# Performance work log

Measured on AMD Instinct MI355X. Metric: run time of the kernel, lower is better.

The kernel has to match this reference:

```python
import jax, jax.numpy as jnp
import numpy as np

P_TH, N_TH, K, NEGPOS = 0.35, 0.4, 10, 7
V0, V1 = 0.1, 0.2


def point_form(b):
    return jnp.concatenate([b[..., :2] - b[..., 2:] / 2, b[..., :2] + b[..., 2:] / 2], -1)


def decode(loc, priors):
    # standard SSD decode, returns cxcywh (point_form is applied by caller)
    cxcy = priors[..., :2] + loc[..., :2] * V0 * priors[..., 2:]
    wh = priors[..., 2:] * jnp.exp(loc[..., 2:] * V1)
    return jnp.concatenate([cxcy, wh], -1)


def jaccard(a, b):
    # a: [N,4], b: [M,4] corner form -> [N,M] IoU
    tl = jnp.maximum(a[:, None, :2], b[None, :, :2])
    br = jnp.minimum(a[:, None, 2:], b[None, :, 2:])
    wh = jnp.clip(br - tl, 0.0)
    inter = wh[..., 0] * wh[..., 1]
    aa = ((a[:, 2] - a[:, 0]) * (a[:, 3] - a[:, 1]))[:, None]
    ab = ((b[:, 2] - b[:, 0]) * (b[:, 3] - b[:, 1]))[None, :]
    return inter / (aa + ab - inter)


def encode(matched, priors):
    g_cxcy = ((matched[..., :2] + matched[..., 2:]) / 2 - priors[..., :2]) / (V0 * priors[..., 2:])
    g_wh = jnp.log((matched[..., 2:] - matched[..., :2]) / priors[..., 2:]) / V1
    return jnp.concatenate([g_cxcy, g_wh], -1)


def encode_landm(matched, priors):
    m = matched.reshape(matched.shape[:-1] + (5, 2))
    g = (m - priors[..., None, :2]) / (V0 * priors[..., None, 2:])
    return g.reshape(matched.shape[:-1] + (10,))


def match_one(truths, loc_single, priors):
    # sequential per-object topk selection with column invalidation (as in original match())
    A = priors.shape[0]
    O = truths.shape[0]
    dec_pf = point_form(decode(jax.lax.stop_gradient(loc_single), priors))
    iou_a = jaccard(truths, point_form(priors))  # [O, A]
    iou_p = jaccard(truths, dec_pf)              # [O, A]

    def step(carry, i):
        iou_a, iou_p = carry
        va, ia = jax.lax.top_k(iou_a[i], K)
        av = va > P_TH
        av = jnp.where(av.any(), av, jnp.arange(K) == 0)  # fallback: best anchor
        ma = jnp.zeros(A, jnp.int32).at[ia].add(av.astype(jnp.int32)) > 0
        iou_a = jnp.where(ma[None, :], -1.0, iou_a)
        iou_p = jnp.where(ma[None, :], -1.0, iou_p)
        vp, ip = jax.lax.top_k(iou_p[i], K)
        pv = vp > P_TH + 0.05
        mp = jnp.zeros(A, jnp.int32).at[ip].add(pv.astype(jnp.int32)) > 0
        iou_a = jnp.where(mp[None, :], -1.0, iou_a)
        iou_p = jnp.where(mp[None, :], -1.0, iou_p)
        return (iou_a, iou_p), (ia, av, ip, pv)

    (iou_a, iou_p), (ia, av, ip, pv) = jax.lax.scan(step, (iou_a, iou_p), jnp.arange(O))
    p_idx = jnp.concatenate([ia, ip], 1).reshape(-1)    # [O*2K]
    p_valid = jnp.concatenate([av, pv], 1).reshape(-1)  # [O*2K] bool
    maxv = jnp.maximum(iou_a, iou_p).max(0)             # max over cat(IoU_A, IoU_P)
    neg_mask = (maxv != -1.0) & (maxv < N_TH)
    pos_mask = jnp.zeros(A, jnp.int32).at[p_idx].add(p_valid.astype(jnp.int32)) > 0
    conf = jnp.full(A, -2.0)
    conf = jnp.where(pos_mask, 1.0, conf)
    conf = jnp.where(neg_mask, 0.0, conf)
    return p_idx, p_valid, conf


def _smooth_l1(d):
    ad = jnp.abs(d)
    return jnp.where(ad < 1.0, 0.5 * d * d, ad - 0.5)


def reference(loc_data, conf_data, landm_data, priors, targets):
    B, A, _ = loc_data.shape
    O = targets.shape[1]
    truths = targets[..., :4]
    landms = targets[..., 4:14]
    labels = targets[..., 14]

    p_idx, p_valid, conf = jax.vmap(match_one, in_axes=(0, 0, None))(truths, loc_data, priors)
    p_true = jnp.repeat(jnp.arange(O), 2 * K)  # object id per match slot

    gat = jax.vmap(lambda x, i: x[i])
    pri_sel = priors[p_idx]            # [B, P, 4]
    tru_sel = truths[:, p_true, :]     # [B, P, 4]
    landm_sel = landms[:, p_true, :]   # [B, P, 10]
    lab_sel = labels[:, p_true]        # [B, P]

    # localization loss
    loc_p = gat(loc_data, p_idx)                       # [B, P, 4]
    loc_t = encode(tru_sel, pri_sel)
    wf = p_valid.astype(loc_data.dtype)
    loss_l = jnp.sum(_smooth_l1(loc_p - loc_t) * wf[..., None])
    N = jnp.sum(p_valid)

    # landmark loss (only label==1 positives, first 6 landm dims)
    lvalid = p_valid & (lab_sel == 1.0)
    landm_p = gat(landm_data, p_idx)                   # [B, P, 6]
    landm_t = encode_landm(landm_sel, pri_sel)[..., :6]
    loss_landm = jnp.sum(_smooth_l1(landm_p - landm_t) * lvalid.astype(loc_data.dtype)[..., None])
    N1 = jnp.sum(lvalid)

    # classification with hard negative mining
    lse = jax.nn.logsumexp(conf_data, axis=-1)         # [B, A]
    pos = conf == 1.0
    n_pos = pos.sum(1)                                  # [B]
    loss_pos = jnp.sum((lse - conf_data[..., 1]) * pos)
    negc = conf == 0.0
    loss_c = lse - conf_data[..., 0]                    # CE with label 0
    masked = jnp.where(negc, loss_c, -jnp.inf)
    order = jnp.argsort(-masked, axis=1)
    rank = jnp.argsort(order, axis=1)
    neg_sel = (rank < (n_pos * NEGPOS)[:, None]) & negc
    loss_neg = jnp.sum(loss_c * neg_sel)
    loss_cls = loss_pos + loss_neg

    return loss_l / N, loss_cls / N, loss_landm / N1


def setup_inputs() -> dict:
    key = jax.random.key(0)
    ks = jax.random.split(key, 8)
    B, A, O = 16, 65536, 24
    loc_data = jax.random.normal(ks[0], (B, A, 4), jnp.float32) * 0.1
    conf_data = jax.random.normal(ks[1], (B, A, 2), jnp.float32)
    landm_data = jax.random.normal(ks[2], (B, A, 6), jnp.float32)
    # priors: cxcywh in unit square with positive wh
    pc = jax.random.uniform(ks[3], (A, 2), jnp.float32, 0.05, 0.95)
    pwh = jax.random.uniform(ks[4], (A, 2), jnp.float32, 0.02, 0.2)
    priors = jnp.concatenate([pc, pwh], 1)
    # targets: valid corner-form boxes + 10 landm coords + label 1
    tc = jax.random.uniform(ks[5], (B, O, 2), jnp.float32, 0.15, 0.85)
    twh = jax.random.uniform(ks[6], (B, O, 2), jnp.float32, 0.05, 0.25)
    boxes = jnp.concatenate([tc - twh / 2, tc + twh / 2], -1)
    lm = jax.random.uniform(ks[7], (B, O, 10), jnp.float32)
    lab = jnp.ones((B, O, 1), jnp.float32)
    targets = jnp.concatenate([boxes, lm, lab], -1)
    return {"loc_data": loc_data, "conf_data": conf_data, "landm_data": landm_data, "priors": priors, "targets": targets}
```

## Files before the change

### kernel.cpp

```cpp
#include <hip/hip_runtime.h>

#define A_N 65536
#define B_N 16
#define O_N 24
#define KEEP 512
#define SELCAP 2048
#define PF 4

typedef unsigned long long u64;

__device__ __forceinline__ float sl1(float d){
  float ad = fabsf(d);
  return ad < 1.0f ? 0.5f * d * d : ad - 0.5f;
}

__device__ __forceinline__ float iou_box(float ax1, float ay1, float ax2, float ay2,
                                         float bx1, float by1, float bx2, float by2){
  float tlx = fmaxf(ax1, bx1), tly = fmaxf(ay1, by1);
  float brx = fminf(ax2, bx2), bry = fminf(ay2, by2);
  float w = fmaxf(brx - tlx, 0.0f), h = fmaxf(bry - tly, 0.0f);
  float inter = w * h;
  float aa = (ax2 - ax1) * (ay2 - ay1);
  float ab = (bx2 - bx1) * (by2 - by1);
  return inter / (aa + ab - inter);
}

__global__ __launch_bounds__(256) void prep_kernel(const float* __restrict__ loc,
    const float* __restrict__ priors, float4* __restrict__ dec,
    float4* __restrict__ pf, unsigned char* __restrict__ flags){
  const int a = blockIdx.x * 256 + threadIdx.x;
  const int b = blockIdx.y;
  const float4 pr = ((const float4*)priors)[a];
  const float4 l = ((const float4*)loc)[(size_t)b * A_N + a];
  float cx = pr.x + l.x * 0.1f * pr.z;
  float cy = pr.y + l.y * 0.1f * pr.w;
  float w  = pr.z * expf(l.z * 0.2f);
  float h  = pr.w * expf(l.w * 0.2f);
  float4 d;
  d.x = cx - w * 0.5f; d.y = cy - h * 0.5f;
  d.z = cx + w * 0.5f; d.w = cy + h * 0.5f;
  dec[(size_t)b * A_N + a] = d;
  if (b == 0){
    float4 p;
    p.x = pr.x - pr.z * 0.5f; p.y = pr.y - pr.w * 0.5f;
    p.z = pr.x + pr.z * 0.5f; p.w = pr.y + pr.w * 0.5f;
    pf[a] = p;
  }
  flags[(size_t)b * A_N + a] = 0;
}

__device__ __forceinline__ void wave_sort_512(u64* sk, int base, int lane, bool asc){
  for (int k = 2; k <= 512; k <<= 1){
    for (int j = k >> 1; j > 0; j >>= 1){
      #pragma unroll
      for (int s = 0; s < 8; ++s){
        int t = lane + s * 64;
        int x = t ^ j;
        if (x > t){
          u64 ka = sk[base + t], kb = sk[base + x];
          bool up = (((t & k) == 0) != asc);
          bool sw = up ? (kb > ka) : (ka > kb);
          if (sw){ sk[base + t] = kb; sk[base + x] = ka; }
        }
      }
      __builtin_amdgcn_wave_barrier();
    }
  }
}

__global__ __launch_bounds__(256) void sel_kernel(const float4* __restrict__ dec,
    const float4* __restrict__ pf, const float* __restrict__ targets,
    unsigned char* __restrict__ flags,
    float* __restrict__ out_vals, int* __restrict__ out_idxs){
  __shared__ unsigned hist[2048];
  __shared__ u64 sk[SELCAP];
  __shared__ unsigned gsum_s[64];
  __shared__ int s_b1, s_cnt;
  const int r = blockIdx.x;
  const int type = r & 1;
  const int o = (r >> 1) % O_N;
  const int b = r / (O_N * 2);
  const int tid = threadIdx.x;
  const int w = tid >> 6;
  const int lane = tid & 63;
  const u64 lmask = (1ull << lane) - 1ull;
  const float* tg = targets + (size_t)(b * O_N + o) * 15;
  const float tx1 = tg[0], ty1 = tg[1], tx2 = tg[2], ty2 = tg[3];
  const float4* src = (type == 0) ? pf : (dec + (size_t)b * A_N);
  unsigned char* fl = flags + (size_t)b * A_N;

  for (int j = tid; j < 2048; j += 256) hist[j] = 0u;
  if (tid == 0) s_cnt = 0;
  __syncthreads();

  const int NCH = A_N / 256;
  {
    float4 nxt[PF];
    #pragma unroll
    for (int u = 0; u < PF; ++u) nxt[u] = src[u * 256 + tid];
    for (int c = 0; c < NCH; c += PF){
      float4 cur[PF];
      #pragma unroll
      for (int u = 0; u < PF; ++u) cur[u] = nxt[u];
      if (c + PF < NCH){
        #pragma unroll
        for (int u = 0; u < PF; ++u) nxt[u] = src[(c + PF + u) * 256 + tid];
      }
      #pragma unroll
      for (int u = 0; u < PF; ++u){
        const int a = (c + u) * 256 + tid;
        const float4 bb = cur[u];
        const float v = iou_box(tx1, ty1, tx2, ty2, bb.x, bb.y, bb.z, bb.w);
        if (v >= 0.4f) fl[a] = 1;
        if (v > 0.0f){
          unsigned bin = __float_as_uint(v) >> 19;
          if (bin > 2047u) bin = 2047u;
          atomicAdd(&hist[bin], 1u);
        }
      }
    }
  }
  __syncthreads();
  if (tid < 64){
    unsigned s = 0;
    #pragma unroll
    for (int e = 0; e < 32; ++e) s += hist[tid * 32 + e];
    gsum_s[tid] = s;
  }
  __syncthreads();
  if (tid == 0){
    int cum = 0, b1 = -1;
    for (int g = 63; g >= 0 && b1 < 0; --g){
      unsigned gs = gsum_s[g];
      if (cum + (int)gs >= KEEP){
        for (int bin = g * 32 + 31; bin >= g * 32; --bin){
          cum += (int)hist[bin];
          if (cum >= KEEP){ b1 = bin; break; }
        }
      } else cum += (int)gs;
    }
    s_b1 = (b1 < 0) ? 0 : b1;
  }
  __syncthreads();
  const int b1 = s_b1;
  {
    float4 nxt[PF];
    #pragma unroll
    for (int u = 0; u < PF; ++u) nxt[u] = src[u * 256 + tid];
    for (int c = 0; c < NCH; c += PF){
      float4 cur[PF];
      #pragma unroll
      for (int u = 0; u < PF; ++u) cur[u] = nxt[u];
      if (c + PF < NCH){
        #pragma unroll
        for (int u = 0; u < PF; ++u) nxt[u] = src[(c + PF + u) * 256 + tid];
      }
      #pragma unroll
      for (int u = 0; u < PF; ++u){
        const int a = (c + u) * 256 + tid;
        const float4 bb = cur[u];
        const float v = iou_box(tx1, ty1, tx2, ty2, bb.x, bb.y, bb.z, bb.w);
        unsigned bits = __float_as_uint(v);
        unsigned bin = bits >> 19;
        if (bin > 2047u) bin = 2047u;
        bool acc = (v > 0.0f) && ((int)bin >= b1);
        u64 m = __ballot(acc);
        if (m){
          int base = 0;
          if (lane == 0) base = atomicAdd(&s_cnt, (int)__popcll(m));
          base = __shfl(base, 0);
          if (acc){
            int p = base + (int)__popcll(m & lmask);
            if (p < SELCAP) sk[p] = ((u64)bits << 32) | (u64)(~(unsigned)a);
          }
        }
      }
    }
  }
  __syncthreads();
  int cnt = s_cnt; if (cnt > SELCAP) cnt = SELCAP;
  for (int j = cnt + tid; j < SELCAP; j += 256) sk[j] = 0ull;
  __syncthreads();
  wave_sort_512(sk, w * 512, lane, (w & 1) != 0);
  __syncthreads();
  for (int k = 1024; k <= 2048; k <<= 1){
    for (int j = k >> 1; j > 0; j >>= 1){
      for (int t = tid; t < SELCAP; t += 256){
        int x = t ^ j;
        if (x > t){
          u64 ka = sk[t], kb = sk[x];
          bool up = ((t & k) == 0);
          bool sw = up ? (kb > ka) : (ka > kb);
          if (sw){ sk[t] = kb; sk[x] = ka; }
        }
      }
      __syncthreads();
    }
  }
  for (int jj = tid; jj < KEEP; jj += 256){
    u64 kk = sk[jj];
    out_vals[(size_t)r * KEEP + jj] = __uint_as_float((unsigned)(kk >> 32));
    out_idxs[(size_t)r * KEEP + jj] = (kk == 0ull) ? 0 : (int)(~(unsigned)kk);
  }
}

__global__ __launch_bounds__(64) void scan_kernel(const float* __restrict__ vals,
    const int* __restrict__ idxs, int* __restrict__ p_idx, int* __restrict__ p_valid,
    unsigned int* __restrict__ bitset_g, int* __restrict__ n_pos_g){
  __shared__ unsigned int bs[A_N / 32];
  __shared__ float pv0[48][64];
  __shared__ int pi0[48][64];
  __shared__ float s_v[10];
  __shared__ int s_i[10];
  const int b = blockIdx.x;
  const int lane = threadIdx.x;
  for (int j = lane; j < A_N / 32; j += 64) bs[j] = 0u;
  for (int row = 0; row < 48; ++row){
    pv0[row][lane] = vals[(size_t)(b * 48 + row) * KEEP + lane];
    pi0[row][lane] = idxs[(size_t)(b * 48 + row) * KEEP + lane];
  }
  __syncthreads();
  int npos = 0;
  const float PTH2 = (float)(0.35 + 0.05);
  for (int o = 0; o < O_N; ++o){
    for (int ph = 0; ph < 2; ++ph){
      const int row48 = o * 2 + ph;
      const int r = b * 48 + row48;
      const float* rv = vals + (size_t)r * KEEP;
      const int* ri = idxs + (size_t)r * KEEP;
      int found = 0;
      for (int pos = 0; pos < KEEP && found < 10; pos += 64){
        float v; int id;
        if (pos == 0){ v = pv0[row48][lane]; id = pi0[row48][lane]; }
        else { v = rv[pos + lane]; id = ri[pos + lane]; }
        bool unm = ((bs[id >> 5] >> (id & 31)) & 1u) == 0u;
        unsigned long long m = __ballot(unm);
        int rank = found + __popcll(m & ((1ull << lane) - 1ull));
        if (unm && rank < 10){ s_v[rank] = v; s_i[rank] = id; }
        int add = __popcll(m);
        found = (found + add > 10) ? 10 : (found + add);
        __syncthreads();
      }
      if (lane == 0){
        const float th = (ph == 0) ? 0.35f : PTH2;
        float fv[10]; int fi[10]; int vv[10];
        bool any = false;
        for (int j = 0; j < 10; ++j){
          fv[j] = (j < found) ? s_v[j] : 0.0f;
          fi[j] = (j < found) ? s_i[j] : 0;
          vv[j] = (fv[j] > th) ? 1 : 0;
          any = any || (vv[j] != 0);
        }
        if (ph == 0 && !any) vv[0] = 1;
        int base_slot = b * (O_N * 20) + o * 20 + ph * 10;
        for (int j = 0; j < 10; ++j){
          p_idx[base_slot + j] = fi[j];
          p_valid[base_slot + j] = vv[j];
          if (vv[j]){
            bs[fi[j] >> 5] |= (1u << (fi[j] & 31));
            npos++;
          }
        }
      }
      __syncthreads();
    }
  }
  for (int j = lane; j < A_N / 32; j += 64) bitset_g[b * (A_N / 32) + j] = bs[j];
  if (lane == 0) n_pos_g[b] = npos;
}

__global__ __launch_bounds__(256) void anchor_kernel(const float* __restrict__ conf,
    const unsigned char* __restrict__ flags, const unsigned int* __restrict__ bitset_g,
    float* __restrict__ lossc, float* __restrict__ partial){
  const int b = blockIdx.y;
  const int a = blockIdx.x * 256 + threadIdx.x;
  __shared__ float red[256];
  bool masked = ((bitset_g[b * (A_N / 32) + (a >> 5)] >> (a & 31)) & 1u) != 0u;
  const float2 c = ((const float2*)conf)[(size_t)b * A_N + a];
  float mx = fmaxf(c.x, c.y);
  float lse = mx + log1pf(expf(-fabsf(c.x - c.y)));
  float lp = 0.0f;
  float lc = -1.0f;
  if (masked) lp = lse - c.y;
  else if (!flags[(size_t)b * A_N + a]) lc = lse - c.x;
  lossc[(size_t)b * A_N + a] = lc;
  red[threadIdx.x] = lp; __syncthreads();
  for (int s = 128; s > 0; s >>= 1){
    if (threadIdx.x < s) red[threadIdx.x] += red[threadIdx.x + s];
    __syncthreads();
  }
  if (threadIdx.x == 0) partial[blockIdx.y * gridDim.x + blockIdx.x] = red[0];
}

__global__ __launch_bounds__(512) void mine_kernel(const float* __restrict__ lossc,
    const int* __restrict__ n_pos_g, double* __restrict__ accum){
  __shared__ unsigned hist[8192];
  __shared__ u64 sk[SELCAP];
  __shared__ unsigned gsum_s[256];
  __shared__ int s_b1, s_need, s_cnt;
  __shared__ float red[512];
  const int b = blockIdx.x;
  const int tid = threadIdx.x;
  const int w = tid >> 6;
  const int lane = tid & 63;
  const u64 lmask = (1ull << lane) - 1ull;
  const float4* lc4 = (const float4*)(lossc + (size_t)b * A_N);
  const int M = n_pos_g[b] * 7;
  if (M <= 0) return;
  for (int j = tid; j < 8192; j += 512) hist[j] = 0u;
  if (tid == 0) s_cnt = 0;
  __syncthreads();
  for (int q = tid; q < A_N / 4; q += 512){
    float4 v4 = lc4[q];
    float vv[4] = {v4.x, v4.y, v4.z, v4.w};
    #pragma unroll
    for (int e = 0; e < 4; ++e){
      if (vv[e] >= 0.0f){
        unsigned bin = __float_as_uint(vv[e]) >> 19;
        if (bin > 8191u) bin = 8191u;
        atomicAdd(&hist[bin], 1u);
      }
    }
  }
  __syncthreads();
  if (tid < 256){
    unsigned s = 0;
    #pragma unroll
    for (int e = 0; e < 32; ++e) s += hist[tid * 32 + e];
    gsum_s[tid] = s;
  }
  __syncthreads();
  if (tid == 0){
    int cum = 0, b1 = -1, need = 0;
    for (int g = 255; g >= 0 && b1 < 0; --g){
      unsigned gs = gsum_s[g];
      if (cum + (int)gs >= M){
        for (int bin = g * 32 + 31; bin >= g * 32; --bin){
          int cc = (int)hist[bin];
          if (cum + cc >= M){ b1 = bin; need = M - cum; break; }
          cum += cc;
        }
      } else cum += (int)gs;
    }
    s_b1 = b1;
    s_need = need;
  }
  __syncthreads();
  const int b1 = s_b1;
  const int need = s_need;
  float sum = 0.0f;
  for (int q = tid; q < A_N / 4; q += 512){
    float4 v4 = lc4[q];
    float vv[4] = {v4.x, v4.y, v4.z, v4.w};
    #pragma unroll
    for (int e = 0; e < 4; ++e){
      float v = vv[e];
      bool isneg = (v >= 0.0f);
      unsigned bits = __float_as_uint(v);
      unsigned bin = bits >> 19;
      if (bin > 8191u) bin = 8191u;
      if (isneg && (int)bin > b1) sum += v;
      bool acc = isneg && ((int)bin == b1);
      u64 m = __ballot(acc);
      if (m){
        int base = 0;
        if (lane == 0) base = atomicAdd(&s_cnt, (int)__popcll(m));
        base = __shfl(base, 0);
        if (acc){
          int p = base + (int)__popcll(m & lmask);
          if (p < SELCAP) sk[p] = (u64)bits;
        }
      }
    }
  }
  __syncthreads();
  int cnt = s_cnt; if (cnt > SELCAP) cnt = SELCAP;
  for (int j = cnt + tid; j < SELCAP; j += 512) sk[j] = 0ull;
  __syncthreads();
  if (w < 4) wave_sort_512(sk, w * 512, lane, (w & 1) != 0);
  __syncthreads();
  for (int k = 1024; k <= 2048; k <<= 1){
    for (int j = k >> 1; j > 0; j >>= 1){
      for (int t = tid; t < SELCAP; t += 512){
        int x = t ^ j;
        if (x > t){
          u64 ka = sk[t], kb = sk[x];
          bool up = ((t & k) == 0);
          bool sw = up ? (kb > ka) : (ka > kb);
          if (sw){ sk[t] = kb; sk[x] = ka; }
        }
      }
      __syncthreads();
    }
  }
  for (int i = tid; i < need; i += 512) sum += __uint_as_float((unsigned)sk[i]);
  red[tid] = sum; __syncthreads();
  for (int s = 256; s > 0; s >>= 1){
    if (tid < s) red[tid] += red[tid + s];
    __syncthreads();
  }
  if (tid == 0) atomicAdd(&accum[3], (double)red[0]);
}

__global__ __launch_bounds__(512) void loss_lm_kernel(const float* __restrict__ loc,
    const float* __restrict__ landm, const float* __restrict__ priors,
    const float* __restrict__ targets, const int* __restrict__ p_idx,
    const int* __restrict__ p_valid, double* __restrict__ accum, int* __restrict__ cnts){
  const int b = blockIdx.x;
  const int j = threadIdx.x;
  float ll = 0.0f, lmv = 0.0f;
  int nv = 0, nv1 = 0;
  if (j < 480){
    int valid = p_valid[b * 480 + j];
    if (valid){
      int pid = p_idx[b * 480 + j];
      int t = j / 20;
      const float* tg = targets + (size_t)(b * O_N + t) * 15;
      float4 pr = ((const float4*)priors)[pid];
      float4 lp = ((const float4*)loc)[(size_t)b * A_N + pid];
      float gcx = ((tg[0] + tg[2]) * 0.5f - pr.x) / (0.1f * pr.z);
      float gcy = ((tg[1] + tg[3]) * 0.5f - pr.y) / (0.1f * pr.w);
      float gw = logf((tg[2] - tg[0]) / pr.z) / 0.2f;
      float gh = logf((tg[3] - tg[1]) / pr.w) / 0.2f;
      ll = sl1(lp.x - gcx) + sl1(lp.y - gcy) + sl1(lp.z - gw) + sl1(lp.w - gh);
      nv = 1;
      if (tg[14] == 1.0f){
        nv1 = 1;
        const float* lmp = landm + ((size_t)b * A_N + pid) * 6;
        for (int k = 0; k < 3; ++k){
          float gx = (tg[4 + 2 * k] - pr.x) / (0.1f * pr.z);
          float gy = (tg[5 + 2 * k] - pr.y) / (0.1f * pr.w);
          lmv += sl1(lmp[2 * k] - gx) + sl1(lmp[2 * k + 1] - gy);
        }
      }
    }
  }
  __shared__ float redf[512];
  __shared__ int redi[512];
  redf[j] = ll; __syncthreads();
  for (int s = 256; s > 0; s >>= 1){ if (j < s) redf[j] += redf[j + s]; __syncthreads(); }
  float llT = redf[0]; __syncthreads();
  redf[j] = lmv; __syncthreads();
  for (int s = 256; s > 0; s >>= 1){ if (j < s) redf[j] += redf[j + s]; __syncthreads(); }
  float lmT = redf[0]; __syncthreads();
  redi[j] = nv; __syncthreads();
  for (int s = 256; s > 0; s >>= 1){ if (j < s) redi[j] += redi[j + s]; __syncthreads(); }
  int nT = redi[0]; __syncthreads();
  redi[j] = nv1; __syncthreads();
  for (int s = 256; s > 0; s >>= 1){ if (j < s) redi[j] += redi[j + s]; __syncthreads(); }
  int n1T = redi[0];
  if (j == 0){
    atomicAdd(&accum[0], (double)llT);
    atomicAdd(&accum[1], (double)lmT);
    atomicAdd(&cnts[0], nT);
    atomicAdd(&cnts[1], n1T);
  }
}

__global__ __launch_bounds__(256) void final_kernel(const double* __restrict__ accum,
    const int* __restrict__ cnts, const float* __restrict__ partial, int npart,
    float* __restrict__ out){
  __shared__ double red[256];
  double s = 0.0;
  for (int i = threadIdx.x; i < npart; i += 256) s += (double)partial[i];
  red[threadIdx.x] = s; __syncthreads();
  for (int st = 128; st > 0; st >>= 1){
    if (threadIdx.x < st) red[threadIdx.x] += red[threadIdx.x + st];
    __syncthreads();
  }
  if (threadIdx.x == 0){
    double N = (double)cnts[0];
    double N1 = (double)cnts[1];
    out[0] = (float)(accum[0] / N);
    out[1] = (float)((red[0] + accum[3]) / N);
    out[2] = (float)(accum[1] / N1);
  }
}

extern "C" void kernel_launch(void* const* d_in, const int* in_sizes, int n_in,
                              void* d_out, int out_size, void* d_ws, size_t ws_size,
                              hipStream_t stream){
  (void)in_sizes; (void)n_in; (void)out_size; (void)ws_size;
  const float* loc     = (const float*)d_in[0];
  const float* conf    = (const float*)d_in[1];
  const float* landm   = (const float*)d_in[2];
  const float* priors  = (const float*)d_in[3];
  const float* targets = (const float*)d_in[4];
  float* out = (float*)d_out;
  char* ws = (char*)d_ws;

  double* accum = (double*)ws;
  int* cnts = (int*)(ws + 32);
  size_t off = 64;
  float4* dec = (float4*)(ws + off);  off += (size_t)B_N * A_N * 16;
  float4* pf  = (float4*)(ws + off);  off += (size_t)A_N * 16;
  unsigned char* flags = (unsigned char*)(ws + off); off += (size_t)B_N * A_N;
  float* vals = (float*)(ws + off); off += (size_t)B_N * O_N * 2 * KEEP * 4;
  int* idxs   = (int*)(ws + off);   off += (size_t)B_N * O_N * 2 * KEEP * 4;
  int* p_idx  = (int*)(ws + off);   off += (size_t)B_N * 480 * 4;
  int* p_val  = (int*)(ws + off);   off += (size_t)B_N * 480 * 4;
  unsigned int* bitset = (unsigned int*)(ws + off); off += (size_t)B_N * (A_N / 32) * 4;
  int* n_pos  = (int*)(ws + off);   off += 64;
  float* lossc = (float*)(ws + off); off += (size_t)B_N * A_N * 4;
  float* partial = (float*)(ws + off); off += (size_t)B_N * (A_N / 256) * 4;

  hipMemsetAsync(ws, 0, 64, stream);
  hipLaunchKernelGGL(prep_kernel, dim3(A_N / 256, B_N), dim3(256), 0, stream,
                     loc, priors, dec, pf, flags);
  hipLaunchKernelGGL(sel_kernel, dim3(B_N * O_N * 2), dim3(256), 0, stream,
                     dec, pf, targets, flags, vals, idxs);
  hipLaunchKernelGGL(scan_kernel, dim3(B_N), dim3(64), 0, stream,
                     vals, idxs, p_idx, p_val, bitset, n_pos);
  hipLaunchKernelGGL(anchor_kernel, dim3(A_N / 256, B_N), dim3(256), 0, stream,
                     conf, flags, bitset, lossc, partial);
  hipLaunchKernelGGL(mine_kernel, dim3(B_N), dim3(512), 0, stream,
                     lossc, n_pos, accum);
  hipLaunchKernelGGL(loss_lm_kernel, dim3(B_N), dim3(512), 0, stream,
                     loc, landm, priors, targets, p_idx, p_val, accum, cnts);
  hipLaunchKernelGGL(final_kernel, dim3(1), dim3(256), 0, stream,
                     accum, cnts, partial, B_N * (A_N / 256), out);
}
```

Baseline: 457.4 us.

## Replace two-pass histogram top-k selection with overlap prefilter and single candidate pass

The selection kernel now makes one pass over anchors. Each wave queues only the anchors whose box overlaps the target, then computes IoU for those anchors alone, sets the flags, and collects candidates above a 0.1 pre-threshold into a larger shared buffer before a bitonic sort. The earlier full-histogram two-pass method is kept as a fallback for when the candidate count falls below KEEP or overflows the buffer. The target area is hoisted out of the IoU, and the mining kernel is widened to 1024 threads. The cost is more shared memory, a gathered reload of queued anchors, and a possibly larger sort, with a risk of falling back to the slower path.

```diff
diff --git a/kernel.cpp b/kernel.cpp
--- a/kernel.cpp
+++ b/kernel.cpp
@@ -4,7 +4,9 @@
 #define B_N 16
 #define O_N 24
 #define KEEP 512
-#define SELCAP 2048
+#define CAND_CAP 4096
+#define QCAP_W 640
+#define PRE_THR 0.1f
 #define PF 4
 
 typedef unsigned long long u64;
@@ -14,13 +16,12 @@
   return ad < 1.0f ? 0.5f * d * d : ad - 0.5f;
 }
 
-__device__ __forceinline__ float iou_box(float ax1, float ay1, float ax2, float ay2,
-                                         float bx1, float by1, float bx2, float by2){
-  float tlx = fmaxf(ax1, bx1), tly = fmaxf(ay1, by1);
-  float brx = fminf(ax2, bx2), bry = fminf(ay2, by2);
+__device__ __forceinline__ float iou_parts(float tx1, float ty1, float tx2, float ty2,
+                                           float aa, float bx1, float by1, float bx2, float by2){
+  float tlx = fmaxf(tx1, bx1), tly = fmaxf(ty1, by1);
+  float brx = fminf(tx2, bx2), bry = fminf(ty2, by2);
   float w = fmaxf(brx - tlx, 0.0f), h = fmaxf(bry - tly, 0.0f);
   float inter = w * h;
-  float aa = (ax2 - ax1) * (ay2 - ay1);
   float ab = (bx2 - bx1) * (by2 - by1);
   return inter / (aa + ab - inter);
 }
@@ -68,14 +69,33 @@
   }
 }
 
+__device__ __forceinline__ void wave_sort_1024(u64* sk, int base, int lane, bool asc){
+  for (int k = 2; k <= 1024; k <<= 1){
+    for (int j = k >> 1; j > 0; j >>= 1){
+      #pragma unroll
+      for (int s = 0; s < 16; ++s){
+        int t = lane + s * 64;
+        int x = t ^ j;
+        if (x > t){
+          u64 ka = sk[base + t], kb = sk[base + x];
+          bool up = (((t & k) == 0) != asc);
+          bool sw = up ? (kb > ka) : (ka > kb);
+          if (sw){ sk[base + t] = kb; sk[base + x] = ka; }
+        }
+      }
+      __builtin_amdgcn_wave_barrier();
+    }
+  }
+}
+
 __global__ __launch_bounds__(256) void sel_kernel(const float4* __restrict__ dec,
     const float4* __restrict__ pf, const float* __restrict__ targets,
     unsigned char* __restrict__ flags,
     float* __restrict__ out_vals, int* __restrict__ out_idxs){
+  __shared__ u64 cand[CAND_CAP];
+  __shared__ unsigned qbuf[4][QCAP_W];
   __shared__ unsigned hist[2048];
-  __shared__ u64 sk[SELCAP];
-  __shared__ unsigned gsum_s[64];
-  __shared__ int s_b1, s_cnt;
+  __shared__ int s_candCnt, s_b1;
   const int r = blockIdx.x;
   const int type = r & 1;
   const int o = (r >> 1) % O_N;
@@ -86,119 +106,180 @@
   const u64 lmask = (1ull << lane) - 1ull;
   const float* tg = targets + (size_t)(b * O_N + o) * 15;
   const float tx1 = tg[0], ty1 = tg[1], tx2 = tg[2], ty2 = tg[3];
+  const float aa = (tx2 - tx1) * (ty2 - ty1);
   const float4* src = (type == 0) ? pf : (dec + (size_t)b * A_N);
   unsigned char* fl = flags + (size_t)b * A_N;
-
-  for (int j = tid; j < 2048; j += 256) hist[j] = 0u;
-  if (tid == 0) s_cnt = 0;
-  __syncthreads();
-
-  const int NCH = A_N / 256;
-  {
-    float4 nxt[PF];
+  unsigned* myq = qbuf[w];
+
+  if (tid == 0) s_candCnt = 0;
+  __syncthreads();
+
+  int qcnt = 0;
+  const int abase = w * (A_N / 4);
+  const int NCH = (A_N / 4) / 64;
+  float4 nxt[PF];
+  #pragma unroll
+  for (int u = 0; u < PF; ++u) nxt[u] = src[abase + u * 64 + lane];
+  for (int c = 0; c < NCH; c += PF){
+    float4 cur[PF];
     #pragma unroll
-    for (int u = 0; u < PF; ++u) nxt[u] = src[u * 256 + tid];
-    for (int c = 0; c < NCH; c += PF){
-      float4 cur[PF];
+    for (int u = 0; u < PF; ++u) cur[u] = nxt[u];
+    if (c + PF < NCH){
       #pragma unroll
-      for (int u = 0; u < PF; ++u) cur[u] = nxt[u];
-      if (c + PF < NCH){
-        #pragma unroll
-        for (int u = 0; u < PF; ++u) nxt[u] = src[(c + PF + u) * 256 + tid];
-      }
-      #pragma unroll
-      for (int u = 0; u < PF; ++u){
-        const int a = (c + u) * 256 + tid;
-        const float4 bb = cur[u];
-        const float v = iou_box(tx1, ty1, tx2, ty2, bb.x, bb.y, bb.z, bb.w);
-        if (v >= 0.4f) fl[a] = 1;
-        if (v > 0.0f){
-          unsigned bin = __float_as_uint(v) >> 19;
-          if (bin > 2047u) bin = 2047u;
-          atomicAdd(&hist[bin], 1u);
-        }
-      }
-    }
-  }
-  __syncthreads();
-  if (tid < 64){
-    unsigned s = 0;
+      for (int u = 0; u < PF; ++u) nxt[u] = src[abase + (c + PF + u) * 64 + lane];
+    }
     #pragma unroll
-    for (int e = 0; e < 32; ++e) s += hist[tid * 32 + e];
-    gsum_s[tid] = s;
-  }
-  __syncthreads();
-  if (tid == 0){
-    int cum = 0, b1 = -1;
-    for (int g = 63; g >= 0 && b1 < 0; --g){
-      unsigned gs = gsum_s[g];
-      if (cum + (int)gs >= KEEP){
-        for (int bin = g * 32 + 31; bin >= g * 32; --bin){
-          cum += (int)hist[bin];
-          if (cum >= KEEP){ b1 = bin; break; }
-        }
-      } else cum += (int)gs;
-    }
-    s_b1 = (b1 < 0) ? 0 : b1;
-  }
-  __syncthreads();
-  const int b1 = s_b1;
-  {
-    float4 nxt[PF];
-    #pragma unroll
-    for (int u = 0; u < PF; ++u) nxt[u] = src[u * 256 + tid];
-    for (int c = 0; c < NCH; c += PF){
-      float4 cur[PF];
-      #pragma unroll
-      for (int u = 0; u < PF; ++u) cur[u] = nxt[u];
-      if (c + PF < NCH){
-        #pragma unroll
-        for (int u = 0; u < PF; ++u) nxt[u] = src[(c + PF + u) * 256 + tid];
-      }
-      #pragma unroll
-      for (int u = 0; u < PF; ++u){
-        const int a = (c + u) * 256 + tid;
-        const float4 bb = cur[u];
-        const float v = iou_box(tx1, ty1, tx2, ty2, bb.x, bb.y, bb.z, bb.w);
-        unsigned bits = __float_as_uint(v);
-        unsigned bin = bits >> 19;
-        if (bin > 2047u) bin = 2047u;
-        bool acc = (v > 0.0f) && ((int)bin >= b1);
+    for (int u = 0; u < PF; ++u){
+      const int a = abase + (c + u) * 64 + lane;
+      const float4 bb = cur[u];
+      bool ov = (fminf(tx2, bb.z) > fmaxf(tx1, bb.x)) && (fminf(ty2, bb.w) > fmaxf(ty1, bb.y));
+      u64 m = __ballot(ov);
+      if (ov) myq[qcnt + (int)__popcll(m & lmask)] = (unsigned)a;
+      qcnt += (int)__popcll(m);
+    }
+    if (qcnt > QCAP_W - PF * 64){
+      int trips = (qcnt + 63) >> 6;
+      int a0 = 0; float4 cb;
+      if (lane < qcnt){ a0 = (int)myq[lane]; cb = src[a0]; }
+      for (int tr = 0; tr < trips; ++tr){
+        int i = tr * 64 + lane;
+        bool valid = i < qcnt;
+        int a1 = 0; float4 nb;
+        int i2 = i + 64;
+        if (i2 < qcnt){ a1 = (int)myq[i2]; nb = src[a1]; }
+        float v = valid ? iou_parts(tx1, ty1, tx2, ty2, aa, cb.x, cb.y, cb.z, cb.w) : 0.0f;
+        if (valid && v >= 0.4f) fl[a0] = 1;
+        bool acc = valid && (v > PRE_THR);
         u64 m = __ballot(acc);
         if (m){
           int base = 0;
-          if (lane == 0) base = atomicAdd(&s_cnt, (int)__popcll(m));
+          if (lane == 0) base = atomicAdd(&s_candCnt, (int)__popcll(m));
           base = __shfl(base, 0);
           if (acc){
             int p = base + (int)__popcll(m & lmask);
-            if (p < SELCAP) sk[p] = ((u64)bits << 32) | (u64)(~(unsigned)a);
+            if (p < CAND_CAP) cand[p] = ((u64)__float_as_uint(v) << 32) | (u64)(~(unsigned)a0);
           }
         }
-      }
-    }
-  }
-  __syncthreads();
-  int cnt = s_cnt; if (cnt > SELCAP) cnt = SELCAP;
-  for (int j = cnt + tid; j < SELCAP; j += 256) sk[j] = 0ull;
-  __syncthreads();
-  wave_sort_512(sk, w * 512, lane, (w & 1) != 0);
-  __syncthreads();
-  for (int k = 1024; k <= 2048; k <<= 1){
-    for (int j = k >> 1; j > 0; j >>= 1){
-      for (int t = tid; t < SELCAP; t += 256){
-        int x = t ^ j;
-        if (x > t){
-          u64 ka = sk[t], kb = sk[x];
-          bool up = ((t & k) == 0);
-          bool sw = up ? (kb > ka) : (ka > kb);
-          if (sw){ sk[t] = kb; sk[x] = ka; }
-        }
-      }
-      __syncthreads();
+        a0 = a1; cb = nb;
+      }
+      qcnt = 0;
+    }
+  }
+  {
+    int trips = (qcnt + 63) >> 6;
+    int a0 = 0; float4 cb;
+    if (lane < qcnt){ a0 = (int)myq[lane]; cb = src[a0]; }
+    for (int tr = 0; tr < trips; ++tr){
+      int i = tr * 64 + lane;
+      bool valid = i < qcnt;
+      int a1 = 0; float4 nb;
+      int i2 = i + 64;
+      if (i2 < qcnt){ a1 = (int)myq[i2]; nb = src[a1]; }
+      float v = valid ? iou_parts(tx1, ty1, tx2, ty2, aa, cb.x, cb.y, cb.z, cb.w) : 0.0f;
+      if (valid && v >= 0.4f) fl[a0] = 1;
+      bool acc = valid && (v > PRE_THR);
+      u64 m = __ballot(acc);
+      if (m){
+        int base = 0;
+        if (lane == 0) base = atomicAdd(&s_candCnt, (int)__popcll(m));
+        base = __shfl(base, 0);
+        if (acc){
+          int p = base + (int)__popcll(m & lmask);
+          if (p < CAND_CAP) cand[p] = ((u64)__float_as_uint(v) << 32) | (u64)(~(unsigned)a0);
+        }
+      }
+      a0 = a1; cb = nb;
+    }
+  }
+  __syncthreads();
+  int tot = s_candCnt;
+  if (tot < KEEP || tot > CAND_CAP){
+    for (int j = tid; j < 2048; j += 256) hist[j] = 0u;
+    if (tid == 0) s_candCnt = 0;
+    __syncthreads();
+    for (int a = tid; a < A_N; a += 256){
+      float4 bb = src[a];
+      float v = iou_parts(tx1, ty1, tx2, ty2, aa, bb.x, bb.y, bb.z, bb.w);
+      if (v > 0.0f){
+        unsigned bin = __float_as_uint(v) >> 19;
+        if (bin > 2047u) bin = 2047u;
+        atomicAdd(&hist[bin], 1u);
+      }
+    }
+    __syncthreads();
+    if (tid == 0){
+      int cum = 0, b1 = -1;
+      for (int bin = 2047; bin >= 0; --bin){
+        cum += (int)hist[bin];
+        if (cum >= KEEP){ b1 = bin; break; }
+      }
+      s_b1 = (b1 < 0) ? 0 : b1;
+    }
+    __syncthreads();
+    const int b1 = s_b1;
+    for (int a = tid; a < A_N; a += 256){
+      float4 bb = src[a];
+      float v = iou_parts(tx1, ty1, tx2, ty2, aa, bb.x, bb.y, bb.z, bb.w);
+      unsigned bits = __float_as_uint(v);
+      unsigned bin = bits >> 19;
+      if (bin > 2047u) bin = 2047u;
+      bool acc = (v > 0.0f) && ((int)bin >= b1);
+      u64 m = __ballot(acc);
+      if (m){
+        int base = 0;
+        if (lane == 0) base = atomicAdd(&s_candCnt, (int)__popcll(m));
+        base = __shfl(base, 0);
+        if (acc){
+          int p = base + (int)__popcll(m & lmask);
+          if (p < CAND_CAP) cand[p] = ((u64)bits << 32) | (u64)(~(unsigned)a);
+        }
+      }
+    }
+    __syncthreads();
+    tot = s_candCnt;
+    if (tot > CAND_CAP) tot = CAND_CAP;
+  }
+  if (tot <= 2048){
+    for (int j = tot + tid; j < 2048; j += 256) cand[j] = 0ull;
+    __syncthreads();
+    wave_sort_512(cand, w * 512, lane, (w & 1) != 0);
+    __syncthreads();
+    for (int k = 1024; k <= 2048; k <<= 1){
+      for (int j = k >> 1; j > 0; j >>= 1){
+        for (int t = tid; t < 2048; t += 256){
+          int x = t ^ j;
+          if (x > t){
+            u64 ka = cand[t], kb = cand[x];
+            bool up = ((t & k) == 0);
+            bool sw = up ? (kb > ka) : (ka > kb);
+            if (sw){ cand[t] = kb; cand[x] = ka; }
+          }
+        }
+        __syncthreads();
+      }
+    }
+  } else {
+    for (int j = tot + tid; j < CAND_CAP; j += 256) cand[j] = 0ull;
+    __syncthreads();
+    wave_sort_1024(cand, w * 1024, lane, (w & 1) != 0);
+    __syncthreads();
+    for (int k = 2048; k <= 4096; k <<= 1){
+      for (int j = k >> 1; j > 0; j >>= 1){
+        for (int t = tid; t < 4096; t += 256){
+          int x = t ^ j;
+          if (x > t){
+            u64 ka = cand[t], kb = cand[x];
+            bool up = ((t & k) == 0);
+            bool sw = up ? (kb > ka) : (ka > kb);
+            if (sw){ cand[t] = kb; cand[x] = ka; }
+          }
+        }
+        __syncthreads();
+      }
     }
   }
   for (int jj = tid; jj < KEEP; jj += 256){
-    u64 kk = sk[jj];
+    u64 kk = cand[jj];
     out_vals[(size_t)r * KEEP + jj] = __uint_as_float((unsigned)(kk >> 32));
     out_idxs[(size_t)r * KEEP + jj] = (kk == 0ull) ? 0 : (int)(~(unsigned)kk);
   }
@@ -292,13 +373,13 @@
   if (threadIdx.x == 0) partial[blockIdx.y * gridDim.x + blockIdx.x] = red[0];
 }
 
-__global__ __launch_bounds__(512) void mine_kernel(const float* __restrict__ lossc,
+__global__ __launch_bounds__(1024) void mine_kernel(const float* __restrict__ lossc,
     const int* __restrict__ n_pos_g, double* __restrict__ accum){
   __shared__ unsigned hist[8192];
-  __shared__ u64 sk[SELCAP];
+  __shared__ u64 sk[2048];
   __shared__ unsigned gsum_s[256];
   __shared__ int s_b1, s_need, s_cnt;
-  __shared__ float red[512];
+  __shared__ float red[1024];
   const int b = blockIdx.x;
   const int tid = threadIdx.x;
   const int w = tid >> 6;
@@ -307,10 +388,10 @@
   const float4* lc4 = (const float4*)(lossc + (size_t)b * A_N);
   const int M = n_pos_g[b] * 7;
   if (M <= 0) return;
-  for (int j = tid; j < 8192; j += 512) hist[j] = 0u;
+  for (int j = tid; j < 8192; j += 1024) hist[j] = 0u;
   if (tid == 0) s_cnt = 0;
   __syncthreads();
-  for (int q = tid; q < A_N / 4; q += 512){
+  for (int q = tid; q < A_N / 4; q += 1024){
     float4 v4 = lc4[q];
     float vv[4] = {v4.x, v4.y, v4.z, v4.w};
     #pragma unroll
@@ -349,7 +430,7 @@
   const int b1 = s_b1;
   const int need = s_need;
   float sum = 0.0f;
-  for (int q = tid; q < A_N / 4; q += 512){
+  for (int q = tid; q < A_N / 4; q += 1024){
     float4 v4 = lc4[q];
     float vv[4] = {v4.x, v4.y, v4.z, v4.w};
     #pragma unroll
@@ -368,20 +449,20 @@
         base = __shfl(base, 0);
         if (acc){
           int p = base + (int)__popcll(m & lmask);
-          if (p < SELCAP) sk[p] = (u64)bits;
-        }
-      }
-    }
-  }
-  __syncthreads();
-  int cnt = s_cnt; if (cnt > SELCAP) cnt = SELCAP;
-  for (int j = cnt + tid; j < SELCAP; j += 512) sk[j] = 0ull;
+          if (p < 2048) sk[p] = (u64)bits;
+        }
+      }
+    }
+  }
+  __syncthreads();
+  int cnt = s_cnt; if (cnt > 2048) cnt = 2048;
+  for (int j = cnt + tid; j < 2048; j += 1024) sk[j] = 0ull;
   __syncthreads();
   if (w < 4) wave_sort_512(sk, w * 512, lane, (w & 1) != 0);
   __syncthreads();
   for (int k = 1024; k <= 2048; k <<= 1){
     for (int j = k >> 1; j > 0; j >>= 1){
-      for (int t = tid; t < SELCAP; t += 512){
+      for (int t = tid; t < 2048; t += 1024){
         int x = t ^ j;
         if (x > t){
           u64 ka = sk[t], kb = sk[x];
@@ -393,9 +474,9 @@
       __syncthreads();
     }
   }
-  for (int i = tid; i < need; i += 512) sum += __uint_as_float((unsigned)sk[i]);
+  for (int i = tid; i < need; i += 1024) sum += __uint_as_float((unsigned)sk[i]);
   red[tid] = sum; __syncthreads();
-  for (int s = 256; s > 0; s >>= 1){
+  for (int s = 512; s > 0; s >>= 1){
     if (tid < s) red[tid] += red[tid + s];
     __syncthreads();
   }
@@ -513,7 +594,7 @@
                      vals, idxs, p_idx, p_val, bitset, n_pos);
   hipLaunchKernelGGL(anchor_kernel, dim3(A_N / 256, B_N), dim3(256), 0, stream,
                      conf, flags, bitset, lossc, partial);
-  hipLaunchKernelGGL(mine_kernel, dim3(B_N), dim3(512), 0, stream,
+  hipLaunchKernelGGL(mine_kernel, dim3(B_N), dim3(1024), 0, stream,
                      lossc, n_pos, accum);
   hipLaunchKernelGGL(loss_lm_kernel, dim3(B_N), dim3(512), 0, stream,
                      loc, landm, priors, targets, p_idx, p_val, accum, cnts);
```

After: 463.9 us. Within noise of the previous version (+1.4%).
